# Performance work log

Measured on AMD Instinct MI355X. Metric: run time of the kernel, lower is better.

Reference implementation:

```python
import jax, jax.numpy as jnp
import numpy as np
import math

B, N, E = 32, 512, 8192          # graphs, nodes/graph, edges/graph
IN_DIM, D, H, HD, L, C = 64, 128, 4, 32, 3, 10
HID = 2 * D                      # _FeatureMLP hidden = max(d, 2*d)


def _ln(x, g, b, eps=1e-5):
    mu = x.mean(-1, keepdims=True)
    var = ((x - mu) ** 2).mean(-1, keepdims=True)
    return (x - mu) / jnp.sqrt(var + eps) * g + b


def _gelu(x):
    return jax.nn.gelu(x, approximate=False)  # torch nn.GELU default (erf)


def setup_inputs() -> dict:
    key = jax.random.key(0)
    ks = iter(jax.random.split(key, 48))
    def w(*shape):
        return jax.random.normal(next(ks), shape, jnp.float32) * 0.02
    z = lambda *s: jnp.zeros(s, jnp.float32)
    o = lambda *s: jnp.ones(s, jnp.float32)
    return {
        'x': jax.random.normal(next(ks), (B * N, IN_DIM), jnp.float32),
        'src': jax.random.randint(next(ks), (B, E), 0, N),
        'dst': jax.random.randint(next(ks), (B, E), 0, N),
        # node encoder: Linear -> LN -> GELU -> Linear -> LN
        'enc_w1': w(IN_DIM, HID), 'enc_b1': z(HID), 'enc_g1': o(HID), 'enc_bn1': z(HID),
        'enc_w2': w(HID, D), 'enc_b2': z(D), 'enc_g2': o(D), 'enc_bn2': z(D),
        # per-layer edge-message MLP (stacked over L)
        'msg_w1': w(L, 2 * D, D), 'msg_b1': z(L, D),
        'msg_w2': w(L, D, D), 'msg_b2': z(L, D),
        'msg_g': o(L, D), 'msg_bb': z(L, D),
        # per-layer attention
        'qw': w(L, D, H * HD), 'qb': z(L, H * HD),
        'kw': w(L, D, H * HD), 'kb': z(L, H * HD),
        'vw': w(L, D, H * HD), 'vb': z(L, H * HD),
        'ow': w(L, H * HD, D), 'ob': z(L, D),
        'attn_g': o(L, D), 'attn_b': z(L, D),
        # graph head: Linear(4d,2d) -> GELU -> LN -> Linear(2d,C)
        'gh_w1': w(4 * D, 2 * D), 'gh_b1': z(2 * D),
        'gh_g': o(2 * D), 'gh_bn': z(2 * D),
        'gh_w2': w(2 * D, C), 'gh_b2': z(C),
    }


def reference(x, src, dst, enc_w1, enc_b1, enc_g1, enc_bn1, enc_w2, enc_b2, enc_g2, enc_bn2,
              msg_w1, msg_b1, msg_w2, msg_b2, msg_g, msg_bb,
              qw, qb, kw, kb, vw, vb, ow, ob, attn_g, attn_b,
              gh_w1, gh_b1, gh_g, gh_bn, gh_w2, gh_b2):
    # node encoder
    t = _ln(x @ enc_w1 + enc_b1, enc_g1, enc_bn1)
    h = _ln(_gelu(t) @ enc_w2 + enc_b2, enc_g2, enc_bn2)
    h = h.reshape(B, N, D)
    seg = jax.vmap(lambda m, d: jax.ops.segment_sum(m, d, num_segments=N))
    for l in range(L):
        # edge message block: gather src/dst, MLP, scatter-add to dst
        hs = jnp.take_along_axis(h, src[..., None], axis=1)   # [B,E,D]
        hd = jnp.take_along_axis(h, dst[..., None], axis=1)   # [B,E,D]
        m = _gelu(jnp.concatenate([hs, hd], -1) @ msg_w1[l] + msg_b1[l]) @ msg_w2[l] + msg_b2[l]
        h = _ln(h + seg(m, dst), msg_g[l], msg_bb[l])
        # masked attention block (dense per-graph attention)
        q = (h @ qw[l] + qb[l]).reshape(B, N, H, HD)
        k = (h @ kw[l] + kb[l]).reshape(B, N, H, HD)
        v = (h @ vw[l] + vb[l]).reshape(B, N, H, HD)
        scores = jnp.einsum('bnhd,bmhd->bhnm', q, k) / math.sqrt(HD)
        attn = jax.nn.softmax(scores, axis=-1)
        o = jnp.einsum('bhnm,bmhd->bnhd', attn, v).reshape(B, N, H * HD)
        h = _ln(h + o @ ow[l] + ob[l], attn_g[l], attn_b[l])
    # graph pooling: mean | sum | max | std
    mean = h.mean(1)
    summ = h.sum(1)
    mx = h.max(1)
    std = jnp.sqrt(jax.nn.relu((h ** 2).mean(1) - mean ** 2) + 1e-6)
    pool = jnp.concatenate([mean, summ, mx, std], -1)         # [B,4D]
    g = _ln(_gelu(pool @ gh_w1 + gh_b1), gh_g, gh_bn)
    return g @ gh_w2 + gh_b2                                   # [B,C]
```

## Files before the change

### kernel.cpp

```cpp
#include <hip/hip_runtime.h>
#include <cmath>

#define B_   32
#define N_   512
#define E_   8192
#define BN_  16384
#define D_   128

typedef short bf16x8 __attribute__((ext_vector_type(8)));
typedef float f32x4  __attribute__((ext_vector_type(4)));

static __device__ __forceinline__ float bf2f(unsigned short u){
  union{unsigned int i; float f;} v; v.i = ((unsigned int)u)<<16; return v.f;
}
static __device__ __forceinline__ unsigned short f2bf(float f){
  union{unsigned int i; float f;} v; v.f=f;
  unsigned int x=v.i;
  return (unsigned short)((x + 0x7fffu + ((x>>16)&1u))>>16);
}
static __device__ __forceinline__ unsigned int pack2(float a, float b){
  return (unsigned int)f2bf(a) | ((unsigned int)f2bf(b)<<16);
}
static __device__ __forceinline__ float gelu_f(float x){
  float xs=x*0.70710678118654752f;
  float ax=fabsf(xs);
  float t=__builtin_amdgcn_rcpf(1.0f+0.3275911f*ax);
  float p=t*(0.254829592f+t*(-0.284496736f+t*(1.421413741f+t*(-1.453152027f+t*1.061405429f))));
  float er=1.0f - p*__expf(-ax*ax);
  er = (xs<0.f)? -er : er;
  return 0.5f*x*(1.0f+er);
}
static __device__ __forceinline__ float gelu_t(float x){
  float x2=x*x;
  float y=x*(-1.5957691216f + x2*(-0.0713548162f));
  float e=__expf(y);
  return x*__builtin_amdgcn_rcpf(1.0f+e);
}
static __device__ __forceinline__ float ldin(const void* p, size_t i, int isbf){
  return isbf ? bf2f(((const unsigned short*)p)[i]) : ((const float*)p)[i];
}

static __device__ __forceinline__ void block_sum2(float a, float b, float&A, float&Bv, float* red, int nw){
  int lane=threadIdx.x&63, w=threadIdx.x>>6;
  #pragma unroll
  for(int o=32;o>0;o>>=1){ a+=__shfl_down(a,o); b+=__shfl_down(b,o); }
  if(lane==0){ red[w]=a; red[8+w]=b; }
  __syncthreads();
  float sa=0.f, sb=0.f;
  for(int i=0;i<nw;i++){ sa+=red[i]; sb+=red[8+i]; }
  __syncthreads();
  A=sa; Bv=sb;
}

__global__ __launch_bounds__(256) void sort_kernel(
  const int* __restrict__ src, const int* __restrict__ dst,
  int* __restrict__ rowptr, unsigned short* __restrict__ ss,
  const unsigned int* __restrict__ xw, int* __restrict__ flag)
{
  int t=threadIdx.x;
  if(blockIdx.x==32){
    if(t<64){
      int cnt=0;
      for(int i=0;i<32;i++){
        unsigned int w=xw[t+64*i];
        float v=bf2f((unsigned short)(w&0xffffu));
        float av=fabsf(v);
        if(v==0.0f || (av>=6e-5f && av<=8.0f)) cnt++;
      }
      #pragma unroll
      for(int o=32;o>0;o>>=1) cnt+=__shfl_down(cnt,o);
      if(t==0) *flag=(cnt>=1024)?1:0;
    }
    return;
  }
  __shared__ int cnts[512];
  __shared__ int offs[512];
  __shared__ int wred[8];
  int g=blockIdx.x;
  for(int i=t;i<512;i+=256) cnts[i]=0;
  __syncthreads();
  const int* dg=dst+(size_t)g*E_;
  for(int e=t;e<E_;e+=256) atomicAdd(&cnts[dg[e]],1);
  __syncthreads();
  int lane=t&63, w=t>>6;
  int c0=cnts[2*t], c1=cnts[2*t+1];
  int mysum=c0+c1;
  int sc=mysum;
  #pragma unroll
  for(int o=1;o<64;o<<=1){ int v=__shfl_up(sc,o); if(lane>=o) sc+=v; }
  if(lane==63) wred[w]=sc;
  __syncthreads();
  int wbase=0;
  for(int i=0;i<w;i++) wbase+=wred[i];
  int excl=wbase+sc-mysum;
  rowptr[g*513+2*t  ]=excl;
  rowptr[g*513+2*t+1]=excl+c0;
  offs[2*t  ]=excl;
  offs[2*t+1]=excl+c0;
  if(t==255) rowptr[g*513+512]=wbase+sc;
  __syncthreads();
  const int* sg=src+(size_t)g*E_;
  unsigned short* ssg=ss+(size_t)g*E_;
  for(int e=t;e<E_;e+=256){
    int d=dg[e];
    int pos=atomicAdd(&offs[d],1);
    ssg[pos]=(unsigned short)sg[e];
  }
}

__global__ __launch_bounds__(256) void prep_kernel(
  const void* __restrict__ msg_w1, const void* __restrict__ msg_w2,
  const void* __restrict__ qw, const void* __restrict__ kw,
  const void* __restrict__ vw, const void* __restrict__ ow,
  const void* __restrict__ qb, const void* __restrict__ kb, const void* __restrict__ vb,
  const void* __restrict__ ob, const void* __restrict__ msg_b1, const void* __restrict__ msg_b2,
  const void* __restrict__ msg_g, const void* __restrict__ msg_bb,
  const void* __restrict__ attn_g, const void* __restrict__ attn_b,
  const void* __restrict__ enc_w1, const void* __restrict__ enc_w2,
  const void* __restrict__ enc_b1, const void* __restrict__ enc_g1, const void* __restrict__ enc_bn1,
  const void* __restrict__ enc_b2, const void* __restrict__ enc_g2, const void* __restrict__ enc_bn2,
  const void* __restrict__ gh_w1, const void* __restrict__ gh_w2,
  const void* __restrict__ gh_b1, const void* __restrict__ gh_g,
  const void* __restrict__ gh_bn, const void* __restrict__ gh_b2,
  unsigned short* __restrict__ w1t, unsigned short* __restrict__ w2k,
  unsigned short* __restrict__ qkvt, unsigned short* __restrict__ owt,
  unsigned short* __restrict__ w1te, unsigned short* __restrict__ w2te,
  unsigned short* __restrict__ ghw1t, unsigned short* __restrict__ ghw2t,
  unsigned short* __restrict__ cb, const int* __restrict__ flag)
{
  int isbf=*flag;
  int job=blockIdx.y;
  int i=blockIdx.x*256+threadIdx.x;
  if(job<3){
    if(i<32768){ int l=job; int k=i>>7, n=i&127; w1t[l*32768 + n*256 + k]=f2bf(ldin(msg_w1,(size_t)l*32768+i,isbf)); }
  } else if(job<6){
    int l=job-3; if(i<16384){ w2k[l*16384 + i]=f2bf(ldin(msg_w2,(size_t)l*16384+i,isbf)); }
  } else if(job<15){
    int r=job-6, l=r/3, which=r%3;
    if(i<16384){ int k=i>>7, n=i&127;
      const void* w=(which==0)?qw:((which==1)?kw:vw);
      qkvt[l*49152 + (which*128+n)*128 + k]=f2bf(ldin(w,(size_t)l*16384+i,isbf)); }
  } else if(job<18){
    int l=job-15; if(i<16384){ int k=i>>7, n=i&127; owt[l*16384 + n*128 + k]=f2bf(ldin(ow,(size_t)l*16384+i,isbf)); }
  } else if(job==18){
    if(i<3840){
      float v;
      if(i<1152){ int l=i/384, j=i%384, which=j>>7, jj=j&127;
        const void* bb=(which==0)?qb:((which==1)?kb:vb);
        v=ldin(bb,(size_t)l*128+jj,isbf);
      } else {
        int i2=i-1152; int r=i2/384; int rem=i2%384;
        const void* s = (r==0)?ob:((r==1)?msg_b1:((r==2)?msg_b2:((r==3)?msg_g:((r==4)?msg_bb:((r==5)?attn_g:attn_b)))));
        v=ldin(s,(size_t)rem,isbf);
      }
      cb[i]=f2bf(v);
    }
  } else if(job==19){
    if(i<1152){
      float v;
      if(i<256)       v=ldin(enc_b1,i,isbf);
      else if(i<512)  v=ldin(enc_g1,i-256,isbf);
      else if(i<768)  v=ldin(enc_bn1,i-512,isbf);
      else if(i<896)  v=ldin(enc_b2,i-768,isbf);
      else if(i<1024) v=ldin(enc_g2,i-896,isbf);
      else            v=ldin(enc_bn2,i-1024,isbf);
      cb[3840+i]=f2bf(v);
    }
  } else if(job==20){
    if(i<16384){ int k=i>>8, n=i&255; w1te[n*64+k]=f2bf(ldin(enc_w1,(size_t)i,isbf)); }
  } else if(job==21){
    if(i<32768){ int k=i>>7, n=i&127; w2te[n*256+k]=f2bf(ldin(enc_w2,(size_t)i,isbf)); }
  } else if(job<26){
    int p=job-22; int j=p*32768+i;
    if(i<32768){ int k=j>>8, n=j&255; ghw1t[n*512+k]=f2bf(ldin(gh_w1,(size_t)j,isbf)); }
  } else {
    if(i<2560){ int k=i/10, n=i%10; ghw2t[n*256+k]=f2bf(ldin(gh_w2,(size_t)i,isbf)); }
    else if(i<2560+778){
      int j=i-2560; float v;
      if(j<256)      v=ldin(gh_b1,j,isbf);
      else if(j<512) v=ldin(gh_g,j-256,isbf);
      else if(j<768) v=ldin(gh_bn,j-512,isbf);
      else           v=ldin(gh_b2,j-768,isbf);
      cb[4992+j]=f2bf(v);
    }
  }
}

__global__ __launch_bounds__(256) void enc_kernel(
  const void* __restrict__ x, const unsigned short* __restrict__ w1te,
  const unsigned short* __restrict__ w2te, const unsigned short* __restrict__ cb,
  unsigned short* __restrict__ h, const int* __restrict__ flag,
  const unsigned short* __restrict__ w1t0, unsigned short* __restrict__ UV)
{
  __shared__ __align__(16) unsigned short xs[64][72];
  __shared__ __align__(16) unsigned short t1[64][264];
  int isbf=*flag;
  int m0=blockIdx.x*64;
  int t=threadIdx.x, lane=t&63, w=t>>6, quad=lane>>4, ln=lane&15;
  for(int c2=t;c2<1024;c2+=256){
    int i=c2*4, row=i>>6, col=i&63;
    float v0,v1,v2,v3;
    if(isbf){
      const unsigned short* p=(const unsigned short*)x+(size_t)m0*64+i;
      v0=bf2f(p[0]); v1=bf2f(p[1]); v2=bf2f(p[2]); v3=bf2f(p[3]);
    } else {
      float4 f=*(const float4*)((const float*)x+(size_t)m0*64+i);
      v0=f.x; v1=f.y; v2=f.z; v3=f.w;
    }
    ushort4 o; o.x=f2bf(v0); o.y=f2bf(v1); o.z=f2bf(v2); o.w=f2bf(v3);
    *(ushort4*)&xs[row][col]=o;
  }
  __syncthreads();
  f32x4 a[4][4];
  #pragma unroll
  for(int nt=0;nt<4;nt++){ a[nt][0]={0,0,0,0}; a[nt][1]={0,0,0,0}; a[nt][2]={0,0,0,0}; a[nt][3]={0,0,0,0}; }
  #pragma unroll
  for(int k0i=0;k0i<2;k0i++){
    bf16x8 af[4];
    #pragma unroll
    for(int f=0;f<4;f++) af[f]=*(const bf16x8*)(&xs[f*16+ln][k0i*32+quad*8]);
    #pragma unroll
    for(int nt=0;nt<4;nt++){
      int n=w*64+nt*16+ln;
      bf16x8 bfr=*(const bf16x8*)(w1te+(size_t)n*64+k0i*32+quad*8);
      #pragma unroll
      for(int f=0;f<4;f++) a[nt][f]=__builtin_amdgcn_mfma_f32_16x16x32_bf16(af[f],bfr,a[nt][f],0,0,0);
    }
  }
  #pragma unroll
  for(int nt=0;nt<4;nt++){
    int n=w*64+nt*16+ln;
    float bv=bf2f(cb[3840+n]);
    #pragma unroll
    for(int f=0;f<4;f++)
      #pragma unroll
      for(int r=0;r<4;r++) t1[f*16+quad*4+r][n]=f2bf(a[nt][f][r]+bv);
  }
  __syncthreads();
  {
    int row=t>>2, qq=t&3;
    float s=0.f,s2=0.f;
    for(int c=qq*64;c<qq*64+64;c++){ float v=bf2f(t1[row][c]); s+=v; s2+=v*v; }
    s+=__shfl_xor(s,1); s+=__shfl_xor(s,2);
    s2+=__shfl_xor(s2,1); s2+=__shfl_xor(s2,2);
    float mu=s*(1.f/256.f), var=fmaxf(s2*(1.f/256.f)-mu*mu,0.f);
    float rr=rsqrtf(var+1e-5f);
    for(int c=qq*64;c<qq*64+64;c++){
      float v=bf2f(t1[row][c]);
      t1[row][c]=f2bf(gelu_f((v-mu)*rr*bf2f(cb[4096+c])+bf2f(cb[4352+c])));
    }
  }
  __syncthreads();
  f32x4 b2a[2][4];
  #pragma unroll
  for(int nt=0;nt<2;nt++){ b2a[nt][0]={0,0,0,0}; b2a[nt][1]={0,0,0,0}; b2a[nt][2]={0,0,0,0}; b2a[nt][3]={0,0,0,0}; }
  #pragma unroll
  for(int k0i=0;k0i<8;k0i++){
    bf16x8 af[4];
    #pragma unroll
    for(int f=0;f<4;f++) af[f]=*(const bf16x8*)(&t1[f*16+ln][k0i*32+quad*8]);
    #pragma unroll
    for(int nt=0;nt<2;nt++){
      int n=w*32+nt*16+ln;
      bf16x8 bfr=*(const bf16x8*)(w2te+(size_t)n*256+k0i*32+quad*8);
      #pragma unroll
      for(int f=0;f<4;f++) b2a[nt][f]=__builtin_amdgcn_mfma_f32_16x16x32_bf16(af[f],bfr,b2a[nt][f],0,0,0);
    }
  }
  __syncthreads();
  float* mf=(float*)&t1[0][0];
  #pragma unroll
  for(int nt=0;nt<2;nt++){
    int n=w*32+nt*16+ln;
    float bv=bf2f(cb[4608+n]);
    #pragma unroll
    for(int f=0;f<4;f++)
      #pragma unroll
      for(int r=0;r<4;r++) mf[(f*16+quad*4+r)*132+n]=b2a[nt][f][r]+bv;
  }
  __syncthreads();
  {
    int row=t>>2, qq=t&3;
    float vals[32];
    float s=0.f,s2=0.f;
    for(int j=0;j<32;j++){ float v=mf[row*132+qq*32+j]; vals[j]=v; s+=v; s2+=v*v; }
    s+=__shfl_xor(s,1); s+=__shfl_xor(s,2);
    s2+=__shfl_xor(s2,1); s2+=__shfl_xor(s2,2);
    float mu=s*(1.f/128.f), var=fmaxf(s2*(1.f/128.f)-mu*mu,0.f);
    float rr=rsqrtf(var+1e-5f);
    for(int j=0;j<32;j+=2){
      int c=qq*32+j;
      float v0=(vals[j]  -mu)*rr*bf2f(cb[4736+c  ])+bf2f(cb[4864+c  ]);
      float v1=(vals[j+1]-mu)*rr*bf2f(cb[4736+c+1])+bf2f(cb[4864+c+1]);
      *(unsigned int*)(h+(size_t)(m0+row)*128+c)=pack2(v0,v1);
      vals[j]=v0; vals[j+1]=v1;
    }
    __syncthreads();
    unsigned short* hb=&t1[0][0];
    for(int j=0;j<32;j++) hb[row*136+qq*32+j]=f2bf(vals[j]);
  }
  __syncthreads();
  {
    const unsigned short* hb=&t1[0][0];
    #pragma unroll
    for(int y=0;y<2;y++)
    #pragma unroll
    for(int nt=0;nt<2;nt++){
      int n=w*32+nt*16+ln;
      f32x4 a0={0,0,0,0},a1={0,0,0,0},a2={0,0,0,0},a3={0,0,0,0};
      const unsigned short* wp=w1t0+(size_t)n*256+y*128+quad*8;
      #pragma unroll
      for(int k0=0;k0<128;k0+=32){
        bf16x8 bfr=*(const bf16x8*)(wp+k0);
        bf16x8 f0=*(const bf16x8*)(hb+(size_t)(ln   )*136+k0+quad*8);
        bf16x8 f1=*(const bf16x8*)(hb+(size_t)(16+ln)*136+k0+quad*8);
        bf16x8 f2=*(const bf16x8*)(hb+(size_t)(32+ln)*136+k0+quad*8);
        bf16x8 f3=*(const bf16x8*)(hb+(size_t)(48+ln)*136+k0+quad*8);
        a0=__builtin_amdgcn_mfma_f32_16x16x32_bf16(f0,bfr,a0,0,0,0);
        a1=__builtin_amdgcn_mfma_f32_16x16x32_bf16(f1,bfr,a1,0,0,0);
        a2=__builtin_amdgcn_mfma_f32_16x16x32_bf16(f2,bfr,a2,0,0,0);
        a3=__builtin_amdgcn_mfma_f32_16x16x32_bf16(f3,bfr,a3,0,0,0);
      }
      float bv=y?0.f:bf2f(cb[1536+n]);
      #pragma unroll
      for(int r=0;r<4;r++){
        UV[(size_t)(m0   +quad*4+r)*256+y*128+n]=f2bf(a0[r]+bv);
        UV[(size_t)(m0+16+quad*4+r)*256+y*128+n]=f2bf(a1[r]+bv);
        UV[(size_t)(m0+32+quad*4+r)*256+y*128+n]=f2bf(a2[r]+bv);
        UV[(size_t)(m0+48+quad*4+r)*256+y*128+n]=f2bf(a3[r]+bv);
      }
    }
  }
}

__global__ __launch_bounds__(256) void qkvgen_kernel(
  const unsigned short* __restrict__ hrows, const unsigned short* __restrict__ wqkv,
  const unsigned short* __restrict__ bqkv,
  unsigned short* __restrict__ Qb, unsigned short* __restrict__ Kb,
  unsigned short* __restrict__ Vtb)
{
  __shared__ __align__(16) unsigned short a_t[64][136];
  int t=threadIdx.x;
  int m0=blockIdx.x*64;
  int y=blockIdx.y;
  for(int c=t;c<1024;c+=256){
    int m=c>>4, pp=c&15;
    *(uint4*)&a_t[m][pp*8]=*((const uint4*)(hrows+(size_t)(m0+m)*128)+pp);
  }
  __syncthreads();
  int lane=t&63, w=t>>6, quad=lane>>4, ln=lane&15;
  int gloc=m0>>9, r0=m0&511;
  #pragma unroll
  for(int nt=0;nt<2;nt++){
    int n=w*32+nt*16+ln;
    f32x4 a0={0,0,0,0},a1={0,0,0,0},a2={0,0,0,0},a3={0,0,0,0};
    const unsigned short* wp=wqkv+(size_t)(y*128+n)*128+quad*8;
    #pragma unroll
    for(int k0=0;k0<128;k0+=32){
      bf16x8 bfr=*(const bf16x8*)(wp+k0);
      bf16x8 f0=*(const bf16x8*)(&a_t[ln   ][k0+quad*8]);
      bf16x8 f1=*(const bf16x8*)(&a_t[16+ln][k0+quad*8]);
      bf16x8 f2=*(const bf16x8*)(&a_t[32+ln][k0+quad*8]);
      bf16x8 f3=*(const bf16x8*)(&a_t[48+ln][k0+quad*8]);
      a0=__builtin_amdgcn_mfma_f32_16x16x32_bf16(f0,bfr,a0,0,0,0);
      a1=__builtin_amdgcn_mfma_f32_16x16x32_bf16(f1,bfr,a1,0,0,0);
      a2=__builtin_amdgcn_mfma_f32_16x16x32_bf16(f2,bfr,a2,0,0,0);
      a3=__builtin_amdgcn_mfma_f32_16x16x32_bf16(f3,bfr,a3,0,0,0);
    }
    float bv=bf2f(bqkv[y*128+n]);
    if(y==0){
      const float sc=0.17677669529663689f;
      #pragma unroll
      for(int r=0;r<4;r++){
        Qb[(size_t)(m0   +quad*4+r)*128+n]=f2bf((a0[r]+bv)*sc);
        Qb[(size_t)(m0+16+quad*4+r)*128+n]=f2bf((a1[r]+bv)*sc);
        Qb[(size_t)(m0+32+quad*4+r)*128+n]=f2bf((a2[r]+bv)*sc);
        Qb[(size_t)(m0+48+quad*4+r)*128+n]=f2bf((a3[r]+bv)*sc);
      }
    } else if(y==1){
      #pragma unroll
      for(int r=0;r<4;r++){
        Kb[(size_t)(m0   +quad*4+r)*128+n]=f2bf(a0[r]+bv);
        Kb[(size_t)(m0+16+quad*4+r)*128+n]=f2bf(a1[r]+bv);
        Kb[(size_t)(m0+32+quad*4+r)*128+n]=f2bf(a2[r]+bv);
        Kb[(size_t)(m0+48+quad*4+r)*128+n]=f2bf(a3[r]+bv);
      }
    } else {
      unsigned short* vrow = Vtb + ((size_t)gloc*128+n)*512 + r0 + quad*4;
      ushort4 o;
      o.x=f2bf(a0[0]+bv); o.y=f2bf(a0[1]+bv); o.z=f2bf(a0[2]+bv); o.w=f2bf(a0[3]+bv);
      *(ushort4*)(vrow)=o;
      o.x=f2bf(a1[0]+bv); o.y=f2bf(a1[1]+bv); o.z=f2bf(a1[2]+bv); o.w=f2bf(a1[3]+bv);
      *(ushort4*)(vrow+16)=o;
      o.x=f2bf(a2[0]+bv); o.y=f2bf(a2[1]+bv); o.z=f2bf(a2[2]+bv); o.w=f2bf(a2[3]+bv);
      *(ushort4*)(vrow+32)=o;
      o.x=f2bf(a3[0]+bv); o.y=f2bf(a3[1]+bv); o.z=f2bf(a3[2]+bv); o.w=f2bf(a3[3]+bv);
      *(ushort4*)(vrow+48)=o;
    }
  }
}

__global__ __launch_bounds__(128) void edgef_kernel(
  unsigned short* __restrict__ h,
  const unsigned short* __restrict__ UV,
  const unsigned short* __restrict__ ss,
  const int* __restrict__ rowptr,
  const unsigned short* __restrict__ w2k,
  const unsigned short* __restrict__ b2,
  const unsigned short* __restrict__ gg, const unsigned short* __restrict__ bbp,
  int b0, int gEp)
{
  __shared__ __align__(16) float aggL[2][4][128];
  __shared__ __align__(16) float po[2][4][128];
  int t=threadIdx.x, lane=t&63, w=t>>6;
  int bid=blockIdx.x;
  int lg=bid%gEp, ch=bid/gEp;
  int g=b0+lg;
  const unsigned short* UVg = UV + (size_t)g*512*256;
  const unsigned short* ssg = ss + (size_t)g*E_;
  int dbase = ch*4;
  int bnd[5];
  #pragma unroll
  for(int i=0;i<5;i++) bnd[i]=rowptr[g*513+dbase+i];
  #pragma unroll 1
  for(int dd=0;dd<4;dd++){
    int e_lo=bnd[dd], e_hi0=bnd[dd+1];
    int half=(e_hi0-e_lo+1)>>1;
    int es = w ? (e_lo+half) : e_lo;
    int ee = w ? e_hi0       : (e_lo+half);
    unsigned int vdw=*(const unsigned int*)(UVg + (size_t)(dbase+dd)*256 + 128 + lane*2);
    float v0=bf2f((unsigned short)(vdw&0xffffu)), v1=bf2f((unsigned short)(vdw>>16));
    float a0=0.f, a1=0.f;
    int si3,si4,si5;
    unsigned int u0,u1,u2;
    {
      int s0=__builtin_amdgcn_readfirstlane((int)ssg[es  ])&511;
      int s1=__builtin_amdgcn_readfirstlane((int)ssg[es+1])&511;
      int s2=__builtin_amdgcn_readfirstlane((int)ssg[es+2])&511;
      si3=(int)ssg[es+3]; si4=(int)ssg[es+4]; si5=(int)ssg[es+5];
      u0=*(const unsigned int*)(UVg + (size_t)s0*256 + lane*2);
      u1=*(const unsigned int*)(UVg + (size_t)s1*256 + lane*2);
      u2=*(const unsigned int*)(UVg + (size_t)s2*256 + lane*2);
    }
    #pragma unroll 2
    for(int e=es;e<ee;e++){
      float z0=bf2f((unsigned short)(u0&0xffffu))+v0;
      float z1=bf2f((unsigned short)(u0>>16))+v1;
      u0=u1; u1=u2;
      int s3=__builtin_amdgcn_readfirstlane(si3)&511;
      u2=*(const unsigned int*)(UVg + (size_t)s3*256 + lane*2);
      si3=si4; si4=si5;
      si5=(int)ssg[e+6];
      a0+=gelu_t(z0); a1+=gelu_t(z1);
    }
    aggL[w][dd][lane*2  ]=a0;
    aggL[w][dd][lane*2+1]=a1;
  }
  __syncthreads();
  float o[4][2];
  #pragma unroll
  for(int dd=0;dd<4;dd++){ o[dd][0]=0.f; o[dd][1]=0.f; }
  #pragma unroll 4
  for(int kk=0;kk<64;kk++){
    int k=w*64+kk;
    unsigned int wdw=*(const unsigned int*)(w2k+(size_t)k*128+lane*2);
    float w0=bf2f((unsigned short)(wdw&0xffffu));
    float w1=bf2f((unsigned short)(wdw>>16));
    #pragma unroll
    for(int dd=0;dd<4;dd++){
      float av=aggL[0][dd][k]+aggL[1][dd][k];
      o[dd][0]+=av*w0; o[dd][1]+=av*w1;
    }
  }
  #pragma unroll
  for(int dd=0;dd<4;dd++){
    po[w][dd][lane*2  ]=o[dd][0];
    po[w][dd][lane*2+1]=o[dd][1];
  }
  __syncthreads();
  #pragma unroll 1
  for(int p=0;p<2;p++){
    int di=w*2+p;
    int d = dbase + di;
    float deg=(float)(bnd[di+1]-bnd[di]);
    float o0=bf2f(b2[lane*2  ])*deg + po[0][di][lane*2  ] + po[1][di][lane*2  ];
    float o1=bf2f(b2[lane*2+1])*deg + po[0][di][lane*2+1] + po[1][di][lane*2+1];
    size_t base=(size_t)(g*512+d)*128;
    unsigned int hdw=*(const unsigned int*)(h+base+lane*2);
    float x0=bf2f((unsigned short)(hdw&0xffffu))+o0;
    float x1=bf2f((unsigned short)(hdw>>16))+o1;
    float s1=x0+x1, s2=x0*x0+x1*x1;
    #pragma unroll
    for(int off=32;off>0;off>>=1){ s1+=__shfl_xor(s1,off); s2+=__shfl_xor(s2,off); }
    float mu=s1*(1.f/128.f), var=fmaxf(s2*(1.f/128.f)-mu*mu,0.f);
    float rr=rsqrtf(var+1e-5f);
    float y0=(x0-mu)*rr*bf2f(gg[lane*2  ])+bf2f(bbp[lane*2  ]);
    float y1=(x1-mu)*rr*bf2f(gg[lane*2+1])+bf2f(bbp[lane*2+1]);
    *(unsigned int*)(h+base+lane*2)=pack2(y0,y1);
  }
}

__global__ __launch_bounds__(256) void attn_fused_kernel(
  const unsigned short* __restrict__ Qb, const unsigned short* __restrict__ Kb,
  const unsigned short* __restrict__ Vtb,
  const unsigned short* __restrict__ wo, const unsigned short* __restrict__ bo,
  unsigned short* __restrict__ h,
  const unsigned short* __restrict__ gg, const unsigned short* __restrict__ bbp,
  const unsigned short* __restrict__ w1tn, const unsigned short* __restrict__ b1n,
  unsigned short* __restrict__ UV, float* part, int b0, int gA, int do_uv)
{
  __shared__ __align__(16) unsigned short hO[32][136];
  __shared__ __align__(16) unsigned short Psh[4][16][72];
  __shared__ __align__(16) float mf[32][132];
  int bx=blockIdx.x;
  int lg=bx%gA, ch=bx/gA;
  int r0=ch*32;
  int g=b0+lg;
  int t=threadIdx.x, lane=t&63, w=t>>6, quad=lane>>4, ln=lane&15;
  const unsigned short* Qg = Qb + (size_t)lg*65536;
  const unsigned short* Kg = Kb + (size_t)lg*65536 + w*32;
  const unsigned short* Vg = Vtb + ((size_t)lg*128 + w*32)*512;
  bf16x8 qf[2];
  #pragma unroll
  for(int qt=0;qt<2;qt++)
    qf[qt]=*(const bf16x8*)(Qg + (size_t)(r0+qt*16+ln)*128 + w*32 + quad*8);
  f32x4 O[2][2]; float Lp[2][4];
  #pragma unroll
  for(int qt=0;qt<2;qt++){ O[qt][0]={0,0,0,0}; O[qt][1]={0,0,0,0};
    #pragma unroll
    for(int r=0;r<4;r++) Lp[qt][r]=0.f; }
  for(int kc=0;kc<8;kc++){
    bf16x8 kf[4];
    #pragma unroll
    for(int f=0;f<4;f++) kf[f]=*(const bf16x8*)(Kg + (size_t)(kc*64+f*16+ln)*128 + quad*8);
    bf16x8 va[2], vb[2];
    #pragma unroll
    for(int s2=0;s2<2;s2++){
      va[s2]=*(const bf16x8*)(Vg + (size_t)ln*512      + kc*64 + s2*32 + quad*8);
      vb[s2]=*(const bf16x8*)(Vg + (size_t)(16+ln)*512 + kc*64 + s2*32 + quad*8);
    }
    #pragma unroll
    for(int qt=0;qt<2;qt++){
      f32x4 s[4];
      #pragma unroll
      for(int f=0;f<4;f++){
        f32x4 z={0,0,0,0};
        s[f]=__builtin_amdgcn_mfma_f32_16x16x32_bf16(qf[qt],kf[f],z,0,0,0);
      }
      #pragma unroll
      for(int f=0;f<4;f++)
        #pragma unroll
        for(int r=0;r<4;r++){
          float pe=__expf(fminf(s[f][r],30.0f));
          Psh[w][quad*4+r][f*16+ln]=f2bf(pe);
          Lp[qt][r]+=pe;
        }
      #pragma unroll
      for(int s2=0;s2<2;s2++){
        bf16x8 pf=*(const bf16x8*)(&Psh[w][ln][s2*32+quad*8]);
        O[qt][0]=__builtin_amdgcn_mfma_f32_16x16x32_bf16(pf,va[s2],O[qt][0],0,0,0);
        O[qt][1]=__builtin_amdgcn_mfma_f32_16x16x32_bf16(pf,vb[s2],O[qt][1],0,0,0);
      }
    }
  }
  #pragma unroll
  for(int qt=0;qt<2;qt++){
    #pragma unroll
    for(int o=1;o<16;o<<=1)
      #pragma unroll
      for(int r=0;r<4;r++) Lp[qt][r]+=__shfl_xor(Lp[qt][r],o);
    #pragma unroll
    for(int r=0;r<4;r++){
      float inv=1.0f/Lp[qt][r];
      int qr=qt*16+quad*4+r;
      hO[qr][w*32+ln   ]=f2bf(O[qt][0][r]*inv);
      hO[qr][w*32+16+ln]=f2bf(O[qt][1][r]*inv);
    }
  }
  __syncthreads();
  #pragma unroll
  for(int nt=0;nt<2;nt++){
    int n=w*32+nt*16+ln;
    f32x4 a0={0,0,0,0},a1={0,0,0,0};
    const unsigned short* wp=wo+(size_t)n*128+quad*8;
    #pragma unroll
    for(int k0=0;k0<128;k0+=32){
      bf16x8 bfr=*(const bf16x8*)(wp+k0);
      bf16x8 f0=*(const bf16x8*)(&hO[ln   ][k0+quad*8]);
      bf16x8 f1=*(const bf16x8*)(&hO[16+ln][k0+quad*8]);
      a0=__builtin_amdgcn_mfma_f32_16x16x32_bf16(f0,bfr,a0,0,0,0);
      a1=__builtin_amdgcn_mfma_f32_16x16x32_bf16(f1,bfr,a1,0,0,0);
    }
    float bv=bf2f(bo[n]);
    #pragma unroll
    for(int r=0;r<4;r++){
      mf[quad*4+r   ][n]=a0[r]+bv;
      mf[16+quad*4+r][n]=a1[r]+bv;
    }
  }
  __syncthreads();
  {
    int row=t>>3, oct=t&7;
    size_t base=((size_t)(g*512+r0+row))*128;
    float vals[16];
    float s=0.f,s2=0.f;
    for(int j=0;j<16;j++){
      int c=oct*16+j;
      float v=bf2f(h[base+c])+mf[row][c];
      vals[j]=v; s+=v; s2+=v*v;
    }
    s+=__shfl_xor(s,1); s+=__shfl_xor(s,2); s+=__shfl_xor(s,4);
    s2+=__shfl_xor(s2,1); s2+=__shfl_xor(s2,2); s2+=__shfl_xor(s2,4);
    float mu=s*(1.f/128.f), var=fmaxf(s2*(1.f/128.f)-mu*mu,0.f);
    float rr=rsqrtf(var+1e-5f);
    for(int j=0;j<16;j+=2){
      int c=oct*16+j;
      float y0=(vals[j]  -mu)*rr*bf2f(gg[c  ])+bf2f(bbp[c  ]);
      float y1=(vals[j+1]-mu)*rr*bf2f(gg[c+1])+bf2f(bbp[c+1]);
      *(unsigned int*)(h+base+c)=pack2(y0,y1);
      hO[row][c]=f2bf(y0); hO[row][c+1]=f2bf(y1);
      mf[row][c]=y0; mf[row][c+1]=y1;
    }
  }
  __syncthreads();
  if(!do_uv){
    if(t<128){
      float s=0.f,s2=0.f,mx=-1e30f;
      for(int r=0;r<32;r++){ float v=mf[r][t]; s+=v; s2+=v*v; mx=fmaxf(mx,v); }
      size_t pb=((size_t)(g*16+ch))*384;
      part[pb+t]=s; part[pb+128+t]=s2; part[pb+256+t]=mx;
    }
    return;
  }
  #pragma unroll
  for(int y=0;y<2;y++)
  #pragma unroll
  for(int nt=0;nt<2;nt++){
    int n=w*32+nt*16+ln;
    f32x4 a0={0,0,0,0},a1={0,0,0,0};
    const unsigned short* wp=w1tn+(size_t)n*256+y*128+quad*8;
    #pragma unroll
    for(int k0=0;k0<128;k0+=32){
      bf16x8 bfr=*(const bf16x8*)(wp+k0);
      bf16x8 f0=*(const bf16x8*)(&hO[ln   ][k0+quad*8]);
      bf16x8 f1=*(const bf16x8*)(&hO[16+ln][k0+quad*8]);
      a0=__builtin_amdgcn_mfma_f32_16x16x32_bf16(f0,bfr,a0,0,0,0);
      a1=__builtin_amdgcn_mfma_f32_16x16x32_bf16(f1,bfr,a1,0,0,0);
    }
    float bv=y?0.f:bf2f(b1n[n]);
    size_t rb=(size_t)(g*512+r0);
    #pragma unroll
    for(int r=0;r<4;r++){
      UV[(rb   +quad*4+r)*256+y*128+n]=f2bf(a0[r]+bv);
      UV[(rb+16+quad*4+r)*256+y*128+n]=f2bf(a1[r]+bv);
    }
  }
}

__global__ __launch_bounds__(256) void head_kernel(
  const float* __restrict__ part, const unsigned short* __restrict__ ghw1t,
  const unsigned short* __restrict__ ghw2t, const unsigned short* __restrict__ cb,
  void* __restrict__ out, const int* __restrict__ flag)
{
  int isbf=*flag;
  int b=blockIdx.x, t=threadIdx.x;
  __shared__ float pl[512];
  __shared__ float gl[256];
  __shared__ float red[16];
  if(t<128){
    float s=0.f,s2=0.f,mx=-1e30f;
    for(int c=0;c<16;c++){
      size_t base=((size_t)(b*16+c))*384;
      s += part[base+t];
      s2+= part[base+128+t];
      mx = fmaxf(mx, part[base+256+t]);
    }
    float mean=s*(1.f/512.f);
    float var=fmaxf(s2*(1.f/512.f)-mean*mean,0.f);
    float sd=sqrtf(var+1e-6f);
    pl[t]=mean; pl[128+t]=s; pl[256+t]=mx; pl[384+t]=sd;
  }
  __syncthreads();
  float a=bf2f(cb[4992+t]);
  const unsigned short* wr=ghw1t+(size_t)t*512;
  for(int k0=0;k0<512;k0+=8){
    bf16x8 wv=*(const bf16x8*)(wr+k0);
    const unsigned short* wp=(const unsigned short*)&wv;
    #pragma unroll
    for(int j=0;j<8;j++) a+=pl[k0+j]*bf2f(wp[j]);
  }
  float u=gelu_f(a);
  float S,S2; block_sum2(u,u*u,S,S2,red,4);
  float mu=S*(1.f/256.f), var=fmaxf(S2*(1.f/256.f)-mu*mu,0.f);
  float r=rsqrtf(var+1e-5f);
  gl[t]=(u-mu)*r*bf2f(cb[5248+t])+bf2f(cb[5504+t]);
  __syncthreads();
  if(t<10){
    float o=bf2f(cb[5760+t]);
    const unsigned short* wr2=ghw2t+(size_t)t*256;
    for(int k0=0;k0<256;k0+=8){
      bf16x8 wv=*(const bf16x8*)(wr2+k0);
      const unsigned short* wp=(const unsigned short*)&wv;
      #pragma unroll
      for(int j=0;j<8;j++) o+=gl[k0+j]*bf2f(wp[j]);
    }
    if(isbf) ((unsigned short*)out)[b*10+t]=f2bf(o);
    else     ((float*)out)[b*10+t]=o;
  }
}

extern "C" void kernel_launch(void* const* d_in, const int* in_sizes, int n_in,
                              void* d_out, int out_size, void* d_ws, size_t ws_size,
                              hipStream_t stream)
{
  const void* x      =d_in[0];
  const int*  src    =(const int*)d_in[1];
  const int*  dstp   =(const int*)d_in[2];
  const void* enc_w1 =d_in[3];  const void* enc_b1 =d_in[4];
  const void* enc_g1 =d_in[5];  const void* enc_bn1=d_in[6];
  const void* enc_w2 =d_in[7];  const void* enc_b2 =d_in[8];
  const void* enc_g2 =d_in[9];  const void* enc_bn2=d_in[10];
  const void* msg_w1 =d_in[11]; const void* msg_b1 =d_in[12];
  const void* msg_w2 =d_in[13]; const void* msg_b2 =d_in[14];
  const void* msg_g  =d_in[15]; const void* msg_bb =d_in[16];
  const void* qw     =d_in[17]; const void* qb     =d_in[18];
  const void* kw     =d_in[19]; const void* kb     =d_in[20];
  const void* vw     =d_in[21]; const void* vb     =d_in[22];
  const void* ow     =d_in[23]; const void* ob     =d_in[24];
  const void* attn_g =d_in[25]; const void* attn_b =d_in[26];
  const void* gh_w1  =d_in[27]; const void* gh_b1  =d_in[28];
  const void* gh_g   =d_in[29]; const void* gh_bn  =d_in[30];
  const void* gh_w2  =d_in[31]; const void* gh_b2  =d_in[32];
  (void)in_sizes; (void)n_in; (void)out_size;

  char* base=(char*)d_ws;
  unsigned short* h    =(unsigned short*)(base);
  unsigned short* w1t  =(unsigned short*)(base + 4194304);
  unsigned short* w2k  =(unsigned short*)(base + 4390912);
  unsigned short* qkvt =(unsigned short*)(base + 4489216);
  unsigned short* owt  =(unsigned short*)(base + 4784128);
  unsigned short* w1te =(unsigned short*)(base + 4882432);
  unsigned short* w2te =(unsigned short*)(base + 4915200);
  unsigned short* ghw1t=(unsigned short*)(base + 4980736);
  unsigned short* ghw2t=(unsigned short*)(base + 5242880);
  unsigned short* cb   =(unsigned short*)(base + 5248000);
  int*   rowptr        =(int*)(base + 5325312);
  int*   flag          =(int*)(base + 5390976);
  unsigned short* ssrt =(unsigned short*)(base + 5505024);
  char* R              = base + 6029312;

  size_t Rcap = (ws_size > 6029312) ? (ws_size - 6029312) : 0;
  int gA = 32;
  while(gA > 4 && 8388608 + (size_t)gA*393216 > Rcap) gA >>= 1;
  int apass = 32/gA;
  unsigned short* UV  =(unsigned short*)R;
  unsigned short* Qb  =UV  + 4194304;
  unsigned short* Kb  =Qb  + (size_t)gA*65536;
  unsigned short* Vtb =Kb  + (size_t)gA*65536;
  float* part=(float*)R;

  sort_kernel<<<33,256,0,stream>>>(src,dstp,rowptr,ssrt,(const unsigned int*)x,flag);
  prep_kernel<<<dim3(128,27),256,0,stream>>>(msg_w1,msg_w2,qw,kw,vw,ow,qb,kb,vb,
      ob,msg_b1,msg_b2,msg_g,msg_bb,attn_g,attn_b,
      enc_w1,enc_w2,enc_b1,enc_g1,enc_bn1,enc_b2,enc_g2,enc_bn2,
      gh_w1,gh_w2,gh_b1,gh_g,gh_bn,gh_b2,
      w1t,w2k,qkvt,owt,w1te,w2te,ghw1t,ghw2t,cb,flag);

  enc_kernel<<<BN_/64,256,0,stream>>>(x,w1te,w2te,cb,h,flag,w1t,UV);

  for(int l=0;l<3;l++){
    edgef_kernel<<<32*128,128,0,stream>>>(h,UV,ssrt,rowptr,
        w2k+(size_t)l*16384, cb+1920+l*128, cb+2304+l*128, cb+2688+l*128, 0, 32);
    int ln=(l+1)%3;
    for(int ap=0;ap<apass;ap++){
      int b0=ap*gA;
      qkvgen_kernel<<<dim3(gA*8,3),256,0,stream>>>(h+(size_t)b0*512*128,
          qkvt+(size_t)l*49152, cb+l*384, Qb, Kb, Vtb);
      attn_fused_kernel<<<gA*16,256,0,stream>>>(Qb, Kb, Vtb,
          owt+(size_t)l*16384, cb+1152+l*128, h, cb+3072+l*128, cb+3456+l*128,
          w1t+(size_t)ln*32768, cb+1536+ln*128, UV, part, b0, gA, (l<2)?1:0);
    }
  }
  head_kernel<<<B_,256,0,stream>>>(part,ghw1t,ghw2t,cb,d_out,flag);
}
```

Measured before the change: 383.3 us.

## Split attention keys across wave pairs, halve qkvgen tiles, pair destinations in edge loop

```diff
diff --git a/kernel.cpp b/kernel.cpp
--- a/kernel.cpp
+++ b/kernel.cpp
@@ -339,11 +339,11 @@
   unsigned short* __restrict__ Qb, unsigned short* __restrict__ Kb,
   unsigned short* __restrict__ Vtb)
 {
-  __shared__ __align__(16) unsigned short a_t[64][136];
+  __shared__ __align__(16) unsigned short a_t[32][136];
   int t=threadIdx.x;
-  int m0=blockIdx.x*64;
+  int m0=blockIdx.x*32;
   int y=blockIdx.y;
-  for(int c=t;c<1024;c+=256){
+  for(int c=t;c<512;c+=256){
     int m=c>>4, pp=c&15;
     *(uint4*)&a_t[m][pp*8]=*((const uint4*)(hrows+(size_t)(m0+m)*128)+pp);
   }
@@ -353,19 +353,15 @@
   #pragma unroll
   for(int nt=0;nt<2;nt++){
     int n=w*32+nt*16+ln;
-    f32x4 a0={0,0,0,0},a1={0,0,0,0},a2={0,0,0,0},a3={0,0,0,0};
+    f32x4 a0={0,0,0,0},a1={0,0,0,0};
     const unsigned short* wp=wqkv+(size_t)(y*128+n)*128+quad*8;
     #pragma unroll
     for(int k0=0;k0<128;k0+=32){
       bf16x8 bfr=*(const bf16x8*)(wp+k0);
       bf16x8 f0=*(const bf16x8*)(&a_t[ln   ][k0+quad*8]);
       bf16x8 f1=*(const bf16x8*)(&a_t[16+ln][k0+quad*8]);
-      bf16x8 f2=*(const bf16x8*)(&a_t[32+ln][k0+quad*8]);
-      bf16x8 f3=*(const bf16x8*)(&a_t[48+ln][k0+quad*8]);
       a0=__builtin_amdgcn_mfma_f32_16x16x32_bf16(f0,bfr,a0,0,0,0);
       a1=__builtin_amdgcn_mfma_f32_16x16x32_bf16(f1,bfr,a1,0,0,0);
-      a2=__builtin_amdgcn_mfma_f32_16x16x32_bf16(f2,bfr,a2,0,0,0);
-      a3=__builtin_amdgcn_mfma_f32_16x16x32_bf16(f3,bfr,a3,0,0,0);
     }
     float bv=bf2f(bqkv[y*128+n]);
     if(y==0){
@@ -374,16 +370,12 @@
       for(int r=0;r<4;r++){
         Qb[(size_t)(m0   +quad*4+r)*128+n]=f2bf((a0[r]+bv)*sc);
         Qb[(size_t)(m0+16+quad*4+r)*128+n]=f2bf((a1[r]+bv)*sc);
-        Qb[(size_t)(m0+32+quad*4+r)*128+n]=f2bf((a2[r]+bv)*sc);
-        Qb[(size_t)(m0+48+quad*4+r)*128+n]=f2bf((a3[r]+bv)*sc);
       }
     } else if(y==1){
       #pragma unroll
       for(int r=0;r<4;r++){
         Kb[(size_t)(m0   +quad*4+r)*128+n]=f2bf(a0[r]+bv);
         Kb[(size_t)(m0+16+quad*4+r)*128+n]=f2bf(a1[r]+bv);
-        Kb[(size_t)(m0+32+quad*4+r)*128+n]=f2bf(a2[r]+bv);
-        Kb[(size_t)(m0+48+quad*4+r)*128+n]=f2bf(a3[r]+bv);
       }
     } else {
       unsigned short* vrow = Vtb + ((size_t)gloc*128+n)*512 + r0 + quad*4;
@@ -392,10 +384,6 @@
       *(ushort4*)(vrow)=o;
       o.x=f2bf(a1[0]+bv); o.y=f2bf(a1[1]+bv); o.z=f2bf(a1[2]+bv); o.w=f2bf(a1[3]+bv);
       *(ushort4*)(vrow+16)=o;
-      o.x=f2bf(a2[0]+bv); o.y=f2bf(a2[1]+bv); o.z=f2bf(a2[2]+bv); o.w=f2bf(a2[3]+bv);
-      *(ushort4*)(vrow+32)=o;
-      o.x=f2bf(a3[0]+bv); o.y=f2bf(a3[1]+bv); o.z=f2bf(a3[2]+bv); o.w=f2bf(a3[3]+bv);
-      *(ushort4*)(vrow+48)=o;
     }
   }
 }
@@ -410,7 +398,7 @@
   const unsigned short* __restrict__ gg, const unsigned short* __restrict__ bbp,
   int b0, int gEp)
 {
-  __shared__ __align__(16) float aggL[2][4][128];
+  __shared__ __align__(16) float aggL[4][128];
   __shared__ __align__(16) float po[2][4][128];
   int t=threadIdx.x, lane=t&63, w=t>>6;
   int bid=blockIdx.x;
@@ -422,39 +410,55 @@
   int bnd[5];
   #pragma unroll
   for(int i=0;i<5;i++) bnd[i]=rowptr[g*513+dbase+i];
-  #pragma unroll 1
-  for(int dd=0;dd<4;dd++){
-    int e_lo=bnd[dd], e_hi0=bnd[dd+1];
-    int half=(e_hi0-e_lo+1)>>1;
-    int es = w ? (e_lo+half) : e_lo;
-    int ee = w ? e_hi0       : (e_lo+half);
-    unsigned int vdw=*(const unsigned int*)(UVg + (size_t)(dbase+dd)*256 + 128 + lane*2);
-    float v0=bf2f((unsigned short)(vdw&0xffffu)), v1=bf2f((unsigned short)(vdw>>16));
-    float a0=0.f, a1=0.f;
-    int si3,si4,si5;
-    unsigned int u0,u1,u2;
+  {
+    int dd0=2*w, dd1=2*w+1;
+    int lo0=bnd[dd0], n0=bnd[dd0+1]-lo0;
+    int lo1=bnd[dd1], n1=bnd[dd1+1]-lo1;
+    int nmax = n0>n1 ? n0 : n1;
+    unsigned int vw0=*(const unsigned int*)(UVg + (size_t)(dbase+dd0)*256 + 128 + lane*2);
+    unsigned int vw1=*(const unsigned int*)(UVg + (size_t)(dbase+dd1)*256 + 128 + lane*2);
+    float v00=bf2f((unsigned short)(vw0&0xffffu)), v01=bf2f((unsigned short)(vw0>>16));
+    float v10=bf2f((unsigned short)(vw1&0xffffu)), v11=bf2f((unsigned short)(vw1>>16));
+    float a00=0.f,a01=0.f,a10=0.f,a11=0.f;
+    int sA3,sA4,sA5, sB3,sB4,sB5;
+    unsigned int uA0,uA1,uA2, uB0,uB1,uB2;
     {
-      int s0=__builtin_amdgcn_readfirstlane((int)ssg[es  ])&511;
-      int s1=__builtin_amdgcn_readfirstlane((int)ssg[es+1])&511;
-      int s2=__builtin_amdgcn_readfirstlane((int)ssg[es+2])&511;
-      si3=(int)ssg[es+3]; si4=(int)ssg[es+4]; si5=(int)ssg[es+5];
-      u0=*(const unsigned int*)(UVg + (size_t)s0*256 + lane*2);
-      u1=*(const unsigned int*)(UVg + (size_t)s1*256 + lane*2);
-      u2=*(const unsigned int*)(UVg + (size_t)s2*256 + lane*2);
-    }
-    #pragma unroll 2
-    for(int e=es;e<ee;e++){
-      float z0=bf2f((unsigned short)(u0&0xffffu))+v0;
-      float z1=bf2f((unsigned short)(u0>>16))+v1;
-      u0=u1; u1=u2;
-      int s3=__builtin_amdgcn_readfirstlane(si3)&511;
-      u2=*(const unsigned int*)(UVg + (size_t)s3*256 + lane*2);
-      si3=si4; si4=si5;
-      si5=(int)ssg[e+6];
-      a0+=gelu_t(z0); a1+=gelu_t(z1);
-    }
-    aggL[w][dd][lane*2  ]=a0;
-    aggL[w][dd][lane*2+1]=a1;
+      int a0i=__builtin_amdgcn_readfirstlane((int)ssg[lo0  ])&511;
+      int a1i=__builtin_amdgcn_readfirstlane((int)ssg[lo0+1])&511;
+      int a2i=__builtin_amdgcn_readfirstlane((int)ssg[lo0+2])&511;
+      sA3=(int)ssg[lo0+3]; sA4=(int)ssg[lo0+4]; sA5=(int)ssg[lo0+5];
+      uA0=*(const unsigned int*)(UVg + (size_t)a0i*256 + lane*2);
+      uA1=*(const unsigned int*)(UVg + (size_t)a1i*256 + lane*2);
+      uA2=*(const unsigned int*)(UVg + (size_t)a2i*256 + lane*2);
+      int b0i=__builtin_amdgcn_readfirstlane((int)ssg[lo1  ])&511;
+      int b1i=__builtin_amdgcn_readfirstlane((int)ssg[lo1+1])&511;
+      int b2i=__builtin_amdgcn_readfirstlane((int)ssg[lo1+2])&511;
+      sB3=(int)ssg[lo1+3]; sB4=(int)ssg[lo1+4]; sB5=(int)ssg[lo1+5];
+      uB0=*(const unsigned int*)(UVg + (size_t)b0i*256 + lane*2);
+      uB1=*(const unsigned int*)(UVg + (size_t)b1i*256 + lane*2);
+      uB2=*(const unsigned int*)(UVg + (size_t)b2i*256 + lane*2);
+    }
+    #pragma unroll 1
+    for(int i=0;i<nmax;i++){
+      float z00=bf2f((unsigned short)(uA0&0xffffu))+v00;
+      float z01=bf2f((unsigned short)(uA0>>16))+v01;
+      float z10=bf2f((unsigned short)(uB0&0xffffu))+v10;
+      float z11=bf2f((unsigned short)(uB0>>16))+v11;
+      uA0=uA1; uA1=uA2;
+      uB0=uB1; uB1=uB2;
+      int sA=__builtin_amdgcn_readfirstlane(sA3)&511;
+      uA2=*(const unsigned int*)(UVg + (size_t)sA*256 + lane*2);
+      sA3=sA4; sA4=sA5; sA5=(int)ssg[lo0+i+6];
+      int sB=__builtin_amdgcn_readfirstlane(sB3)&511;
+      uB2=*(const unsigned int*)(UVg + (size_t)sB*256 + lane*2);
+      sB3=sB4; sB4=sB5; sB5=(int)ssg[lo1+i+6];
+      if(i<n0){ a00+=gelu_t(z00); a01+=gelu_t(z01); }
+      if(i<n1){ a10+=gelu_t(z10); a11+=gelu_t(z11); }
+    }
+    aggL[dd0][lane*2  ]=a00;
+    aggL[dd0][lane*2+1]=a01;
+    aggL[dd1][lane*2  ]=a10;
+    aggL[dd1][lane*2+1]=a11;
   }
   __syncthreads();
   float o[4][2];
@@ -468,7 +472,7 @@
     float w1=bf2f((unsigned short)(wdw>>16));
     #pragma unroll
     for(int dd=0;dd<4;dd++){
-      float av=aggL[0][dd][k]+aggL[1][dd][k];
+      float av=aggL[dd][k];
       o[dd][0]+=av*w0; o[dd][1]+=av*w1;
     }
   }
@@ -500,7 +504,7 @@
   }
 }
 
-__global__ __launch_bounds__(256) void attn_fused_kernel(
+__global__ __launch_bounds__(512) void attn_fused_kernel(
   const unsigned short* __restrict__ Qb, const unsigned short* __restrict__ Kb,
   const unsigned short* __restrict__ Vtb,
   const unsigned short* __restrict__ wo, const unsigned short* __restrict__ bo,
@@ -510,26 +514,28 @@
   unsigned short* __restrict__ UV, float* part, int b0, int gA, int do_uv)
 {
   __shared__ __align__(16) unsigned short hO[32][136];
-  __shared__ __align__(16) unsigned short Psh[4][16][72];
+  __shared__ __align__(16) unsigned short Psh[8][16][72];
+  __shared__ __align__(16) float cmb[4][64][25];
   __shared__ __align__(16) float mf[32][132];
   int bx=blockIdx.x;
   int lg=bx%gA, ch=bx/gA;
   int r0=ch*32;
   int g=b0+lg;
   int t=threadIdx.x, lane=t&63, w=t>>6, quad=lane>>4, ln=lane&15;
+  int hh=w>>1, kh=w&1;
   const unsigned short* Qg = Qb + (size_t)lg*65536;
-  const unsigned short* Kg = Kb + (size_t)lg*65536 + w*32;
-  const unsigned short* Vg = Vtb + ((size_t)lg*128 + w*32)*512;
+  const unsigned short* Kg = Kb + (size_t)lg*65536 + hh*32;
+  const unsigned short* Vg = Vtb + ((size_t)lg*128 + hh*32)*512;
   bf16x8 qf[2];
   #pragma unroll
   for(int qt=0;qt<2;qt++)
-    qf[qt]=*(const bf16x8*)(Qg + (size_t)(r0+qt*16+ln)*128 + w*32 + quad*8);
+    qf[qt]=*(const bf16x8*)(Qg + (size_t)(r0+qt*16+ln)*128 + hh*32 + quad*8);
   f32x4 O[2][2]; float Lp[2][4];
   #pragma unroll
   for(int qt=0;qt<2;qt++){ O[qt][0]={0,0,0,0}; O[qt][1]={0,0,0,0};
     #pragma unroll
     for(int r=0;r<4;r++) Lp[qt][r]=0.f; }
-  for(int kc=0;kc<8;kc++){
+  for(int kc=kh*4;kc<kh*4+4;kc++){
     bf16x8 kf[4];
     #pragma unroll
     for(int f=0;f<4;f++) kf[f]=*(const bf16x8*)(Kg + (size_t)(kc*64+f*16+ln)*128 + quad*8);
@@ -563,24 +569,51 @@
       }
     }
   }
-  #pragma unroll
-  for(int qt=0;qt<2;qt++){
-    #pragma unroll
-    for(int o=1;o<16;o<<=1)
-      #pragma unroll
-      for(int r=0;r<4;r++) Lp[qt][r]+=__shfl_xor(Lp[qt][r],o);
-    #pragma unroll
-    for(int r=0;r<4;r++){
-      float inv=1.0f/Lp[qt][r];
-      int qr=qt*16+quad*4+r;
-      hO[qr][w*32+ln   ]=f2bf(O[qt][0][r]*inv);
-      hO[qr][w*32+16+ln]=f2bf(O[qt][1][r]*inv);
-    }
-  }
-  __syncthreads();
-  #pragma unroll
-  for(int nt=0;nt<2;nt++){
-    int n=w*32+nt*16+ln;
+  __syncthreads();
+  if(kh){
+    float* cp=&cmb[hh][lane][0];
+    #pragma unroll
+    for(int qt=0;qt<2;qt++)
+      #pragma unroll
+      for(int j=0;j<2;j++)
+        #pragma unroll
+        for(int r=0;r<4;r++) cp[qt*8+j*4+r]=O[qt][j][r];
+    #pragma unroll
+    for(int qt=0;qt<2;qt++)
+      #pragma unroll
+      for(int r=0;r<4;r++) cp[16+qt*4+r]=Lp[qt][r];
+  }
+  __syncthreads();
+  if(!kh){
+    const float* cp=&cmb[hh][lane][0];
+    #pragma unroll
+    for(int qt=0;qt<2;qt++)
+      #pragma unroll
+      for(int j=0;j<2;j++)
+        #pragma unroll
+        for(int r=0;r<4;r++) O[qt][j][r]+=cp[qt*8+j*4+r];
+    #pragma unroll
+    for(int qt=0;qt<2;qt++)
+      #pragma unroll
+      for(int r=0;r<4;r++) Lp[qt][r]+=cp[16+qt*4+r];
+    #pragma unroll
+    for(int qt=0;qt<2;qt++){
+      #pragma unroll
+      for(int o=1;o<16;o<<=1)
+        #pragma unroll
+        for(int r=0;r<4;r++) Lp[qt][r]+=__shfl_xor(Lp[qt][r],o);
+      #pragma unroll
+      for(int r=0;r<4;r++){
+        float inv=1.0f/Lp[qt][r];
+        int qr=qt*16+quad*4+r;
+        hO[qr][hh*32+ln   ]=f2bf(O[qt][0][r]*inv);
+        hO[qr][hh*32+16+ln]=f2bf(O[qt][1][r]*inv);
+      }
+    }
+  }
+  __syncthreads();
+  {
+    int n=w*16+ln;
     f32x4 a0={0,0,0,0},a1={0,0,0,0};
     const unsigned short* wp=wo+(size_t)n*128+quad*8;
     #pragma unroll
@@ -599,7 +632,7 @@
     }
   }
   __syncthreads();
-  {
+  if(t<256){
     int row=t>>3, oct=t&7;
     size_t base=((size_t)(g*512+r0+row))*128;
     float vals[16];
@@ -632,27 +665,28 @@
     }
     return;
   }
-  #pragma unroll
-  for(int y=0;y<2;y++)
-  #pragma unroll
-  for(int nt=0;nt<2;nt++){
-    int n=w*32+nt*16+ln;
-    f32x4 a0={0,0,0,0},a1={0,0,0,0};
-    const unsigned short* wp=w1tn+(size_t)n*256+y*128+quad*8;
-    #pragma unroll
-    for(int k0=0;k0<128;k0+=32){
-      bf16x8 bfr=*(const bf16x8*)(wp+k0);
-      bf16x8 f0=*(const bf16x8*)(&hO[ln   ][k0+quad*8]);
-      bf16x8 f1=*(const bf16x8*)(&hO[16+ln][k0+quad*8]);
-      a0=__builtin_amdgcn_mfma_f32_16x16x32_bf16(f0,bfr,a0,0,0,0);
-      a1=__builtin_amdgcn_mfma_f32_16x16x32_bf16(f1,bfr,a1,0,0,0);
-    }
-    float bv=y?0.f:bf2f(b1n[n]);
-    size_t rb=(size_t)(g*512+r0);
-    #pragma unroll
-    for(int r=0;r<4;r++){
-      UV[(rb   +quad*4+r)*256+y*128+n]=f2bf(a0[r]+bv);
-      UV[(rb+16+quad*4+r)*256+y*128+n]=f2bf(a1[r]+bv);
+  {
+    int y=w>>2, nb=(w&3)*32;
+    #pragma unroll
+    for(int nt=0;nt<2;nt++){
+      int n=nb+nt*16+ln;
+      f32x4 a0={0,0,0,0},a1={0,0,0,0};
+      const unsigned short* wp=w1tn+(size_t)n*256+y*128+quad*8;
+      #pragma unroll
+      for(int k0=0;k0<128;k0+=32){
+        bf16x8 bfr=*(const bf16x8*)(wp+k0);
+        bf16x8 f0=*(const bf16x8*)(&hO[ln   ][k0+quad*8]);
+        bf16x8 f1=*(const bf16x8*)(&hO[16+ln][k0+quad*8]);
+        a0=__builtin_amdgcn_mfma_f32_16x16x32_bf16(f0,bfr,a0,0,0,0);
+        a1=__builtin_amdgcn_mfma_f32_16x16x32_bf16(f1,bfr,a1,0,0,0);
+      }
+      float bv=y?0.f:bf2f(b1n[n]);
+      size_t rb=(size_t)(g*512+r0);
+      #pragma unroll
+      for(int r=0;r<4;r++){
+        UV[(rb   +quad*4+r)*256+y*128+n]=f2bf(a0[r]+bv);
+        UV[(rb+16+quad*4+r)*256+y*128+n]=f2bf(a1[r]+bv);
+      }
     }
   }
 }
@@ -774,9 +808,9 @@
     int ln=(l+1)%3;
     for(int ap=0;ap<apass;ap++){
       int b0=ap*gA;
-      qkvgen_kernel<<<dim3(gA*8,3),256,0,stream>>>(h+(size_t)b0*512*128,
+      qkvgen_kernel<<<dim3(gA*16,3),256,0,stream>>>(h+(size_t)b0*512*128,
           qkvt+(size_t)l*49152, cb+l*384, Qb, Kb, Vtb);
-      attn_fused_kernel<<<gA*16,256,0,stream>>>(Qb, Kb, Vtb,
+      attn_fused_kernel<<<gA*16,512,0,stream>>>(Qb, Kb, Vtb,
           owt+(size_t)l*16384, cb+1152+l*128, h, cb+3072+l*128, cb+3456+l*128,
           w1t+(size_t)ln*32768, cb+1536+ln*128, UV, part, b0, gA, (l<2)?1:0);
     }
```

Result: no change. 387.5 us (+1.1%).
